# Kernel optimization log

Hardware: AMD Instinct MI355X
Metric: run time of the kernel (lower is better)

Reference implementation:

```python
import jax, jax.numpy as jnp
import numpy as np

# Dims: B=batch, H=query heads, HKV=kv heads, T=query len, S=cache/key len, Dh=head dim
B, H, HKV, T, S, Dh = 2, 32, 8, 1024, 2048, 128
THRESH = 0.000488  # keep keys whose mean attention (over heads and queries) exceeds this


def setup_inputs() -> dict:
    key = jax.random.key(0)
    k1, k2, k3 = jax.random.split(key, 3)
    # attn_w emulates post-softmax attention probabilities: rows sum to 1 over key axis
    attn_w = jax.random.uniform(k1, (B, H, T, S), dtype=jnp.float32)
    attn_w = attn_w / attn_w.sum(axis=-1, keepdims=True)
    v = jax.random.normal(k2, (B, HKV, S, Dh), dtype=jnp.float32)
    w_o = jax.random.normal(k3, (H * Dh, H * Dh), dtype=jnp.float32) * 0.02  # o_proj weight (no bias, Mistral)
    return {"attn_w": attn_w, "v": v, "w_o": w_o}


def reference(attn_w, v, w_o):
    # keep = attn_w.mean(dim=(1,2)) > thresh  -> [B, S]
    keep = attn_w.mean(axis=(1, 2)) > THRESH
    pruned_weights = attn_w * keep[:, None, None, :].astype(attn_w.dtype)  # [B,H,T,S]
    # repeat_kv: [B,HKV,S,Dh] -> [B,H,S,Dh] via repeat_interleave on head axis
    groups = attn_w.shape[1] // v.shape[1]
    v_full = jnp.repeat(v, groups, axis=1)
    new_ctx = jnp.einsum('bhts,bhsd->bhtd', pruned_weights, v_full)  # [B,H,T,Dh]
    Bn, Hn, Tn, Dn = new_ctx.shape
    new_ctx = new_ctx.transpose(0, 2, 1, 3).reshape(Bn, Tn, Hn * Dn)  # [B,T,H*Dh]
    out = new_ctx @ w_o.T  # o_proj
    return (out, pruned_weights)
```

## Files before the change

kernel.cpp:

```cpp
#include <hip/hip_runtime.h>
#include <hip/hip_bf16.h>

#define B_ 2
#define H_ 32
#define HKV_ 8
#define T_ 1024
#define S_ 2048
#define DH_ 128
#define HD_ 4096
#define NROW_ 32768
#define THRESH_D 0.000488

typedef __attribute__((ext_vector_type(4))) float f32x4;
typedef __attribute__((ext_vector_type(8))) short bf16x8;

__device__ __forceinline__ void gload_lds16(const void* g, void* l) {
  __builtin_amdgcn_global_load_lds(
      (const __attribute__((address_space(1))) void*)g,
      (__attribute__((address_space(3))) void*)l, 16, 0, 0);
}

__global__ void colsum_partial_k(const float* __restrict__ attn,
                                 double* __restrict__ partial) {
  int tid = threadIdx.x;
  int b = blockIdx.z, y = blockIdx.y;
  int s = blockIdx.x * 1024 + tid * 4;
  const float* base = attn + (size_t)(b * NROW_ + y * 128) * S_ + s;
  double a0 = 0.0, a1 = 0.0, a2 = 0.0, a3 = 0.0;
  for (int r = 0; r < 128; ++r) {
    float4 vv = *(const float4*)(base + (size_t)r * S_);
    a0 += vv.x; a1 += vv.y; a2 += vv.z; a3 += vv.w;
  }
  double* o = partial + (size_t)(b * 256 + y) * S_ + s;
  o[0] = a0; o[1] = a1; o[2] = a2; o[3] = a3;
}

__global__ void reduce_keep_k(const double* __restrict__ partial,
                              float* __restrict__ keep) {
  int i = blockIdx.x * 256 + threadIdx.x;
  int b = i >> 11, s = i & (S_ - 1);
  const double* p = partial + (size_t)b * 256 * S_ + s;
  double sum = 0.0;
  for (int y = 0; y < 256; ++y) sum += p[(size_t)y * S_];
  keep[i] = (sum * (1.0 / 32768.0) > THRESH_D) ? 1.0f : 0.0f;
}

__global__ void convert_v_k(const float* __restrict__ v,
                            __hip_bfloat16* __restrict__ vt) {
  __shared__ float tile[32][33];
  int bh = blockIdx.z;
  int s0 = blockIdx.x * 32, d0 = blockIdx.y * 32;
  const float* vp = v + (size_t)bh * (S_ * DH_);
  __hip_bfloat16* vtp = vt + (size_t)bh * (S_ * DH_);
  int tx = threadIdx.x, ty = threadIdx.y;
  for (int i = 0; i < 32; i += 8)
    tile[ty + i][tx] = vp[(size_t)(s0 + ty + i) * DH_ + d0 + tx];
  __syncthreads();
  int s = s0 + tx;
  for (int i = 0; i < 32; i += 8) {
    int d = d0 + ty + i;
    int ssw = (s & ~63) | ((s ^ ((d & 7) << 3)) & 63);
    vtp[(size_t)d * S_ + ssw] = __float2bfloat16(tile[tx][ty + i]);
  }
}

__global__ void convert_wo_k(const float* __restrict__ w,
                             __hip_bfloat16* __restrict__ wb) {
  size_t idx = ((size_t)blockIdx.x * 256 + threadIdx.x) * 8;
  int n = (int)(idx >> 12);
  int k0 = (int)(idx & (HD_ - 1));
  float4 x = *(const float4*)(w + idx);
  float4 y = *(const float4*)(w + idx + 4);
  union { bf16x8 v8; __hip_bfloat16 h[8]; } u;
  u.h[0] = __float2bfloat16(x.x); u.h[1] = __float2bfloat16(x.y);
  u.h[2] = __float2bfloat16(x.z); u.h[3] = __float2bfloat16(x.w);
  u.h[4] = __float2bfloat16(y.x); u.h[5] = __float2bfloat16(y.y);
  u.h[6] = __float2bfloat16(y.z); u.h[7] = __float2bfloat16(y.w);
  int ksw = (k0 & ~63) | ((k0 ^ ((n & 7) << 3)) & 63);
  *(bf16x8*)(wb + (size_t)n * HD_ + ksw) = u.v8;
}

#define BK1 64
#define NS1 32

__global__ __launch_bounds__(512) void prune_gemm1_k(
    const float* __restrict__ attn, const float* __restrict__ keep,
    const __hip_bfloat16* __restrict__ vt, float* __restrict__ pruned,
    __hip_bfloat16* __restrict__ ctx) {
  __shared__ __align__(16) __hip_bfloat16 As[2][128 * BK1];
  __shared__ __align__(16) __hip_bfloat16 Bs[2][128 * BK1];
  __shared__ float ksh[S_];

  int tid = threadIdx.x;
  int bh = blockIdx.y;
  int b = bh >> 5, h = bh & 31, hkv = h >> 2;
  int t0 = blockIdx.x * 128;
  const float* A = attn + ((size_t)bh * T_ + t0) * S_;
  float* P = pruned + ((size_t)bh * T_ + t0) * S_;
  const __hip_bfloat16* Bv = vt + (size_t)(b * HKV_ + hkv) * (DH_ * S_);
  const float* kp = keep + b * S_;

  int arow = tid >> 2;
  int acol = (tid & 3) * 16;
  int wave = tid >> 6, lane = tid & 63;
  int l16 = lane & 15, lk = lane >> 4;

  f32x4 acc[8];
  f32x4 z = {0.f, 0.f, 0.f, 0.f};
  #pragma unroll
  for (int n = 0; n < 8; ++n) acc[n] = z;

  float4 areg[4];

  {
    int i4 = tid * 4;
    *(float4*)&ksh[i4] = *(const float4*)(kp + i4);
  }

  auto issueA = [&](int ks) {
    const float* ga = A + (size_t)arow * S_ + ks * BK1 + acol;
    #pragma unroll
    for (int j = 0; j < 4; ++j) areg[j] = *(const float4*)(ga + j * 4);
  };

  auto issueB = [&](int ks, int buf) {
    const __hip_bfloat16* g0 = Bv + (size_t)(tid >> 3) * S_ + ks * BK1 + (tid & 7) * 8;
    char* lb = (char*)&Bs[buf][0] + tid * 16;
    gload_lds16(g0, lb);
    gload_lds16(g0 + (size_t)64 * S_, lb + 8192);
  };

  auto stageA = [&](int ks, int buf) {
    float4 p[4];
    #pragma unroll
    for (int j = 0; j < 4; ++j) {
      float4 kv = *(const float4*)&ksh[ks * BK1 + acol + j * 4];
      p[j].x = areg[j].x * kv.x;
      p[j].y = areg[j].y * kv.y;
      p[j].z = areg[j].z * kv.z;
      p[j].w = areg[j].w * kv.w;
    }
    float* gp = P + (size_t)arow * S_ + ks * BK1 + acol;
    #pragma unroll
    for (int j = 0; j < 4; ++j) *(float4*)(gp + j * 4) = p[j];
    union { bf16x8 v8; __hip_bfloat16 h[8]; } u0, u1;
    const float* pf = (const float*)&p[0];
    #pragma unroll
    for (int j = 0; j < 8; ++j) u0.h[j] = __float2bfloat16(pf[j]);
    #pragma unroll
    for (int j = 0; j < 8; ++j) u1.h[j] = __float2bfloat16(pf[8 + j]);
    char* ab = (char*)&As[buf][0];
    int base0 = arow * 128 + acol * 2;
    int sw = (arow & 7) << 4;
    *(bf16x8*)(ab + (base0 ^ sw)) = u0.v8;
    *(bf16x8*)(ab + ((base0 + 16) ^ sw)) = u1.v8;
  };

  auto mfmaStep = [&](int buf) {
    char* ab = (char*)&As[buf][0];
    char* bb = (char*)&Bs[buf][0];
    #pragma unroll
    for (int kk = 0; kk < 2; ++kk) {
      int kb = kk * 64 + lk * 16;
      int ar = wave * 16 + l16;
      bf16x8 af = *(const bf16x8*)(ab + (ar * 128 + (kb ^ ((ar & 7) << 4))));
      #pragma unroll
      for (int n = 0; n < 8; ++n) {
        int br = n * 16 + l16;
        bf16x8 bf = *(const bf16x8*)(bb + (br * 128 + (kb ^ ((br & 7) << 4))));
        acc[n] = __builtin_amdgcn_mfma_f32_16x16x32_bf16(af, bf, acc[n], 0, 0, 0);
      }
    }
  };

  issueA(0);
  issueB(0, 0);
  __syncthreads();
  stageA(0, 0);
  __syncthreads();
  for (int ks = 0; ks < NS1; ++ks) {
    int cur = ks & 1;
    if (ks + 1 < NS1) {
      issueA(ks + 1);
      issueB(ks + 1, cur ^ 1);
    }
    mfmaStep(cur);
    if (ks + 1 < NS1) stageA(ks + 1, cur ^ 1);
    __syncthreads();
  }

  #pragma unroll
  for (int n = 0; n < 8; ++n)
    #pragma unroll
    for (int r = 0; r < 4; ++r) {
      int trow = t0 + wave * 16 + lk * 4 + r;
      int rowm = b * T_ + trow;
      int kcol = h * DH_ + n * 16 + l16;
      int ksw = (kcol & ~63) | ((kcol ^ ((rowm & 7) << 3)) & 63);
      ctx[(size_t)rowm * HD_ + ksw] = __float2bfloat16(acc[n][r]);
    }
}

#define BK2 64
#define NS2 64

__global__ __launch_bounds__(256) void gemm2_k(
    const __hip_bfloat16* __restrict__ Actx,
    const __hip_bfloat16* __restrict__ Bw,
    float* __restrict__ out) {
  __shared__ __align__(16) __hip_bfloat16 As[2][128 * BK2];
  __shared__ __align__(16) __hip_bfloat16 Bs[2][128 * BK2];
  int tid = threadIdx.x;
  int n0 = blockIdx.x * 128, m0 = blockIdx.y * 128;
  const __hip_bfloat16* Ap = Actx + (size_t)m0 * HD_;
  const __hip_bfloat16* Bp = Bw + (size_t)n0 * HD_;
  int wave = tid >> 6, lane = tid & 63;
  int l16 = lane & 15, lk = lane >> 4;

  f32x4 acc[2][8];
  f32x4 z = {0.f, 0.f, 0.f, 0.f};
  #pragma unroll
  for (int m = 0; m < 2; ++m)
    #pragma unroll
    for (int n = 0; n < 8; ++n) acc[m][n] = z;

  auto issue = [&](int ks, int buf) {
    const __hip_bfloat16* ga = Ap + (size_t)(tid >> 3) * HD_ + ks * BK2 + (tid & 7) * 8;
    const __hip_bfloat16* gb = Bp + (size_t)(tid >> 3) * HD_ + ks * BK2 + (tid & 7) * 8;
    char* la = (char*)&As[buf][0] + tid * 16;
    char* lb = (char*)&Bs[buf][0] + tid * 16;
    #pragma unroll
    for (int i = 0; i < 4; ++i) {
      gload_lds16(ga + (size_t)i * 32 * HD_, la + i * 4096);
      gload_lds16(gb + (size_t)i * 32 * HD_, lb + i * 4096);
    }
  };

  auto mfmaStep = [&](int buf) {
    char* ab = (char*)&As[buf][0];
    char* bb = (char*)&Bs[buf][0];
    #pragma unroll
    for (int kk = 0; kk < 2; ++kk) {
      int kb = kk * 64 + lk * 16;
      bf16x8 af[2];
      #pragma unroll
      for (int m = 0; m < 2; ++m) {
        int ar = wave * 32 + m * 16 + l16;
        af[m] = *(const bf16x8*)(ab + (ar * 128 + (kb ^ ((ar & 7) << 4))));
      }
      #pragma unroll
      for (int n = 0; n < 8; ++n) {
        int br = n * 16 + l16;
        bf16x8 bf = *(const bf16x8*)(bb + (br * 128 + (kb ^ ((br & 7) << 4))));
        #pragma unroll
        for (int m = 0; m < 2; ++m)
          acc[m][n] = __builtin_amdgcn_mfma_f32_16x16x32_bf16(af[m], bf, acc[m][n], 0, 0, 0);
      }
    }
  };

  issue(0, 0);
  __syncthreads();
  for (int ks = 0; ks < NS2; ++ks) {
    int cur = ks & 1;
    if (ks + 1 < NS2) issue(ks + 1, cur ^ 1);
    mfmaStep(cur);
    __syncthreads();
  }

  #pragma unroll
  for (int m = 0; m < 2; ++m)
    #pragma unroll
    for (int n = 0; n < 8; ++n)
      #pragma unroll
      for (int r = 0; r < 4; ++r) {
        int row = m0 + wave * 32 + m * 16 + lk * 4 + r;
        int col = n0 + n * 16 + l16;
        out[(size_t)row * HD_ + col] = acc[m][n][r];
      }
}

extern "C" void kernel_launch(void* const* d_in, const int* in_sizes, int n_in,
                              void* d_out, int out_size, void* d_ws, size_t ws_size,
                              hipStream_t stream) {
  const float* attn = (const float*)d_in[0];
  const float* v = (const float*)d_in[1];
  const float* w_o = (const float*)d_in[2];
  float* out = (float*)d_out;
  float* pruned = out + (size_t)B_ * T_ * HD_;

  char* ws = (char*)d_ws;
  size_t off = 0;
  double* partial = (double*)(ws + off); off += (size_t)B_ * 256 * S_ * 8;
  float* keep = (float*)(ws + off);      off += (size_t)B_ * S_ * 4;
  __hip_bfloat16* vt = (__hip_bfloat16*)(ws + off);
  off += (size_t)B_ * HKV_ * DH_ * S_ * 2;
  __hip_bfloat16* wo = (__hip_bfloat16*)(ws + off);
  off += (size_t)HD_ * HD_ * 2;
  __hip_bfloat16* ctx = (__hip_bfloat16*)(ws + off);
  off += (size_t)B_ * T_ * HD_ * 2;

  colsum_partial_k<<<dim3(2, 256, B_), 256, 0, stream>>>(attn, partial);
  reduce_keep_k<<<dim3((B_ * S_) / 256), 256, 0, stream>>>(partial, keep);
  convert_v_k<<<dim3(S_ / 32, DH_ / 32, B_ * HKV_), dim3(32, 8), 0, stream>>>(v, vt);
  convert_wo_k<<<dim3((HD_ * HD_) / (256 * 8)), 256, 0, stream>>>(w_o, wo);
  prune_gemm1_k<<<dim3(T_ / 128, B_ * H_), 512, 0, stream>>>(attn, keep, vt, pruned, ctx);
  gemm2_k<<<dim3(HD_ / 128, (B_ * T_) / 128), 256, 0, stream>>>(ctx, wo, out);

  (void)in_sizes; (void)n_in; (void)out_size; (void)ws_size;
}
```

Baseline: 543.7 us.

## Retune prune GEMM pipeline, remap block order, widen gemm2 blocks, split keep reduction

The prune+GEMM1 kernel now issues fp32 attention loads two stages ahead, using explicit waitcnt and s_barrier with scheduling barriers in place of __syncthreads, and gains an occupancy hint. Both GEMMs use a 1D grid with a swizzled block-to-tile mapping meant to group blocks that share operands for cache locality. gemm2 moves to 512 threads with one 16-row MFMA tile per wave. The keep reduction splits the 256-row sum across four waves and combines them through LDS. These changes aim to hide memory latency and raise parallelism, but the hand-written vmcnt counts are fragile and halving per-wave work in gemm2 lowers operand reuse.

After: 542.4 us. Within noise of the previous version (-0.2%).

```diff
diff --git a/kernel.cpp b/kernel.cpp
--- a/kernel.cpp
+++ b/kernel.cpp
@@ -13,6 +13,8 @@
 
 typedef __attribute__((ext_vector_type(4))) float f32x4;
 typedef __attribute__((ext_vector_type(8))) short bf16x8;
+
+#define SCHED0() __builtin_amdgcn_sched_barrier(0)
 
 __device__ __forceinline__ void gload_lds16(const void* g, void* l) {
   __builtin_amdgcn_global_load_lds(
@@ -37,12 +39,20 @@
 
 __global__ void reduce_keep_k(const double* __restrict__ partial,
                               float* __restrict__ keep) {
-  int i = blockIdx.x * 256 + threadIdx.x;
-  int b = i >> 11, s = i & (S_ - 1);
-  const double* p = partial + (size_t)b * 256 * S_ + s;
+  __shared__ double sh[4][64];
+  int b = blockIdx.x >> 5;
+  int s0 = (blockIdx.x & 31) * 64;
+  int w = threadIdx.x >> 6, l = threadIdx.x & 63;
+  const double* p = partial + (size_t)b * 256 * S_ + s0 + l;
   double sum = 0.0;
-  for (int y = 0; y < 256; ++y) sum += p[(size_t)y * S_];
-  keep[i] = (sum * (1.0 / 32768.0) > THRESH_D) ? 1.0f : 0.0f;
+  #pragma unroll 8
+  for (int y = 0; y < 64; ++y) sum += p[(size_t)(w * 64 + y) * S_];
+  sh[w][l] = sum;
+  __syncthreads();
+  if (w == 0) {
+    double t = (sh[0][l] + sh[1][l]) + (sh[2][l] + sh[3][l]);
+    keep[b * S_ + s0 + l] = (t * (1.0 / 32768.0) > THRESH_D) ? 1.0f : 0.0f;
+  }
 }
 
 __global__ void convert_v_k(const float* __restrict__ v,
@@ -83,7 +93,7 @@
 #define BK1 64
 #define NS1 32
 
-__global__ __launch_bounds__(512) void prune_gemm1_k(
+__global__ __launch_bounds__(512, 4) void prune_gemm1_k(
     const float* __restrict__ attn, const float* __restrict__ keep,
     const __hip_bfloat16* __restrict__ vt, float* __restrict__ pruned,
     __hip_bfloat16* __restrict__ ctx) {
@@ -92,9 +102,10 @@
   __shared__ float ksh[S_];
 
   int tid = threadIdx.x;
-  int bh = blockIdx.y;
+  int lg = ((blockIdx.x & 7) << 6) | (blockIdx.x >> 3);
+  int bh = lg >> 3;
+  int t0 = (lg & 7) * 128;
   int b = bh >> 5, h = bh & 31, hkv = h >> 2;
-  int t0 = blockIdx.x * 128;
   const float* A = attn + ((size_t)bh * T_ + t0) * S_;
   float* P = pruned + ((size_t)bh * T_ + t0) * S_;
   const __hip_bfloat16* Bv = vt + (size_t)(b * HKV_ + hkv) * (DH_ * S_);
@@ -175,18 +186,31 @@
 
   issueA(0);
   issueB(0, 0);
-  __syncthreads();
+  SCHED0();
+  asm volatile("s_waitcnt lgkmcnt(0)" ::: "memory");
+  SCHED0();
+  __builtin_amdgcn_s_barrier();
+  SCHED0();
   stageA(0, 0);
-  __syncthreads();
+  issueA(1);
+  SCHED0();
+  asm volatile("s_waitcnt vmcnt(8) lgkmcnt(0)" ::: "memory");
+  SCHED0();
+  __builtin_amdgcn_s_barrier();
+  SCHED0();
+
   for (int ks = 0; ks < NS1; ++ks) {
     int cur = ks & 1;
-    if (ks + 1 < NS1) {
-      issueA(ks + 1);
-      issueB(ks + 1, cur ^ 1);
-    }
+    if (ks + 1 < NS1) issueB(ks + 1, cur ^ 1);
+    SCHED0();
+    if (ks + 1 < NS1) stageA(ks + 1, cur ^ 1);
+    if (ks + 2 < NS1) issueA(ks + 2);
     mfmaStep(cur);
-    if (ks + 1 < NS1) stageA(ks + 1, cur ^ 1);
-    __syncthreads();
+    SCHED0();
+    asm volatile("s_waitcnt vmcnt(8) lgkmcnt(0)" ::: "memory");
+    SCHED0();
+    __builtin_amdgcn_s_barrier();
+    SCHED0();
   }
 
   #pragma unroll
@@ -204,36 +228,35 @@
 #define BK2 64
 #define NS2 64
 
-__global__ __launch_bounds__(256) void gemm2_k(
+__global__ __launch_bounds__(512) void gemm2_k(
     const __hip_bfloat16* __restrict__ Actx,
     const __hip_bfloat16* __restrict__ Bw,
     float* __restrict__ out) {
   __shared__ __align__(16) __hip_bfloat16 As[2][128 * BK2];
   __shared__ __align__(16) __hip_bfloat16 Bs[2][128 * BK2];
   int tid = threadIdx.x;
-  int n0 = blockIdx.x * 128, m0 = blockIdx.y * 128;
+  int lg = ((blockIdx.x & 7) << 6) | (blockIdx.x >> 3);
+  int n0 = (lg >> 4) * 128;
+  int m0 = (lg & 15) * 128;
   const __hip_bfloat16* Ap = Actx + (size_t)m0 * HD_;
   const __hip_bfloat16* Bp = Bw + (size_t)n0 * HD_;
   int wave = tid >> 6, lane = tid & 63;
   int l16 = lane & 15, lk = lane >> 4;
 
-  f32x4 acc[2][8];
+  f32x4 acc[8];
   f32x4 z = {0.f, 0.f, 0.f, 0.f};
   #pragma unroll
-  for (int m = 0; m < 2; ++m)
-    #pragma unroll
-    for (int n = 0; n < 8; ++n) acc[m][n] = z;
+  for (int n = 0; n < 8; ++n) acc[n] = z;
 
   auto issue = [&](int ks, int buf) {
     const __hip_bfloat16* ga = Ap + (size_t)(tid >> 3) * HD_ + ks * BK2 + (tid & 7) * 8;
     const __hip_bfloat16* gb = Bp + (size_t)(tid >> 3) * HD_ + ks * BK2 + (tid & 7) * 8;
     char* la = (char*)&As[buf][0] + tid * 16;
     char* lb = (char*)&Bs[buf][0] + tid * 16;
-    #pragma unroll
-    for (int i = 0; i < 4; ++i) {
-      gload_lds16(ga + (size_t)i * 32 * HD_, la + i * 4096);
-      gload_lds16(gb + (size_t)i * 32 * HD_, lb + i * 4096);
-    }
+    gload_lds16(ga, la);
+    gload_lds16(ga + (size_t)64 * HD_, la + 8192);
+    gload_lds16(gb, lb);
+    gload_lds16(gb + (size_t)64 * HD_, lb + 8192);
   };
 
   auto mfmaStep = [&](int buf) {
@@ -242,19 +265,13 @@
     #pragma unroll
     for (int kk = 0; kk < 2; ++kk) {
       int kb = kk * 64 + lk * 16;
-      bf16x8 af[2];
-      #pragma unroll
-      for (int m = 0; m < 2; ++m) {
-        int ar = wave * 32 + m * 16 + l16;
-        af[m] = *(const bf16x8*)(ab + (ar * 128 + (kb ^ ((ar & 7) << 4))));
-      }
+      int ar = wave * 16 + l16;
+      bf16x8 af = *(const bf16x8*)(ab + (ar * 128 + (kb ^ ((ar & 7) << 4))));
       #pragma unroll
       for (int n = 0; n < 8; ++n) {
         int br = n * 16 + l16;
         bf16x8 bf = *(const bf16x8*)(bb + (br * 128 + (kb ^ ((br & 7) << 4))));
-        #pragma unroll
-        for (int m = 0; m < 2; ++m)
-          acc[m][n] = __builtin_amdgcn_mfma_f32_16x16x32_bf16(af[m], bf, acc[m][n], 0, 0, 0);
+        acc[n] = __builtin_amdgcn_mfma_f32_16x16x32_bf16(af, bf, acc[n], 0, 0, 0);
       }
     }
   };
@@ -269,15 +286,13 @@
   }
 
   #pragma unroll
-  for (int m = 0; m < 2; ++m)
-    #pragma unroll
-    for (int n = 0; n < 8; ++n)
-      #pragma unroll
-      for (int r = 0; r < 4; ++r) {
-        int row = m0 + wave * 32 + m * 16 + lk * 4 + r;
-        int col = n0 + n * 16 + l16;
-        out[(size_t)row * HD_ + col] = acc[m][n][r];
-      }
+  for (int n = 0; n < 8; ++n)
+    #pragma unroll
+    for (int r = 0; r < 4; ++r) {
+      int row = m0 + wave * 16 + lk * 4 + r;
+      int col = n0 + n * 16 + l16;
+      out[(size_t)row * HD_ + col] = acc[n][r];
+    }
 }
 
 extern "C" void kernel_launch(void* const* d_in, const int* in_sizes, int n_in,
@@ -301,11 +316,11 @@
   off += (size_t)B_ * T_ * HD_ * 2;
 
   colsum_partial_k<<<dim3(2, 256, B_), 256, 0, stream>>>(attn, partial);
-  reduce_keep_k<<<dim3((B_ * S_) / 256), 256, 0, stream>>>(partial, keep);
+  reduce_keep_k<<<dim3(64), 256, 0, stream>>>(partial, keep);
   convert_v_k<<<dim3(S_ / 32, DH_ / 32, B_ * HKV_), dim3(32, 8), 0, stream>>>(v, vt);
   convert_wo_k<<<dim3((HD_ * HD_) / (256 * 8)), 256, 0, stream>>>(w_o, wo);
-  prune_gemm1_k<<<dim3(T_ / 128, B_ * H_), 512, 0, stream>>>(attn, keep, vt, pruned, ctx);
-  gemm2_k<<<dim3(HD_ / 128, (B_ * T_) / 128), 256, 0, stream>>>(ctx, wo, out);
+  prune_gemm1_k<<<dim3(512), 512, 0, stream>>>(attn, keep, vt, pruned, ctx);
+  gemm2_k<<<dim3(512), 512, 0, stream>>>(ctx, wo, out);
 
   (void)in_sizes; (void)n_in; (void)out_size; (void)ws_size;
 }
```
